# Kernel tuning notes

Hardware: AMD Instinct MI355X
Metric: run time of the kernel (lower is better)

The kernel has to match this reference:

```python
import jax, jax.numpy as jnp
import numpy as np

B, T, D, M, H = 1, 256, 512, 64, 8
HD = D // H              # head_dim = 64
IN = 2 * HD + 2 * M      # crossing_net input dim = 256
HID = D // 2             # crossing_net hidden = 256


def setup_inputs() -> dict:
    key = jax.random.key(0)
    ks = jax.random.split(key, 14)
    s = 0.02
    return {
        "x": jax.random.normal(ks[0], (B, T, D), jnp.float32),
        "coords": jax.random.normal(ks[1], (B, T, M), jnp.float32),
        "Wq": jax.random.normal(ks[2], (D, D), jnp.float32) * s,
        "Wk": jax.random.normal(ks[3], (D, D), jnp.float32) * s,
        "Wv": jax.random.normal(ks[4], (D, D), jnp.float32) * s,
        "Wo": jax.random.normal(ks[5], (D, D), jnp.float32) * s,
        "W1": jax.random.normal(ks[6], (IN, HID), jnp.float32) * s,
        "b1": jnp.zeros((HID,), jnp.float32),
        "W2": jax.random.normal(ks[7], (HID, 2), jnp.float32) * s,
        "b2": jnp.zeros((2,), jnp.float32),
        "W3": jax.random.normal(ks[8], (D, D), jnp.float32) * s,
        "b3": jnp.zeros((D,), jnp.float32),
        "W4": jax.random.normal(ks[9], (D, D), jnp.float32) * s,
        "b4": jnp.zeros((D,), jnp.float32),
    }


def reference(x, coords, Wq, Wk, Wv, Wo, W1, b1, W2, b2, W3, b3, W4, b4):
    b, t, d = x.shape
    m = coords.shape[-1]
    hd = d // H
    # projections -> (B, H, T, HD)
    q = (x @ Wq).reshape(b, t, H, hd).transpose(0, 2, 1, 3)
    k = (x @ Wk).reshape(b, t, H, hd).transpose(0, 2, 1, 3)
    v = (x @ Wv).reshape(b, t, H, hd).transpose(0, 2, 1, 3)
    # crossing_net layer1 on concat([q_i, k_j, c_i, c_j]) decomposes by blocks of W1:
    W1q, W1k = W1[:hd], W1[hd:2 * hd]
    W1ci, W1cj = W1[2 * hd:2 * hd + m], W1[2 * hd + m:]
    a_i = jnp.einsum('bhid,df->bhif', q, W1q) + jnp.einsum('bim,mf->bif', coords, W1ci)[:, None]
    a_j = jnp.einsum('bhjd,df->bhjf', k, W1k) + jnp.einsum('bjm,mf->bjf', coords, W1cj)[:, None] + b1
    # (B,H,T,T,HID) pairwise hidden, then layer2 -> 2 logits
    h = jax.nn.silu(a_i[:, :, :, None, :] + a_j[:, :, None, :, :])
    z = jnp.einsum('bhijf,fc->bhijc', h, W2) + b2
    crossings = jax.nn.softmax(z, axis=-1)            # (B,H,T,T,2)
    linking = crossings[..., 0] - crossings[..., 1]   # (B,H,T,T)
    scores = linking / np.float32(np.sqrt(hd))
    causal = jnp.triu(jnp.ones((t, t), bool), 1)
    scores = jnp.where(causal, -jnp.inf, scores)
    attn = jax.nn.softmax(scores, axis=-1)
    out = jnp.einsum('bhij,bhjd->bhid', attn, v)
    out = out.transpose(0, 2, 1, 3).reshape(b, t, d)
    out = jax.nn.silu(out @ W3 + b3) @ W4 + b4        # invariant_net
    out = out @ Wo                                    # to_out
    writhe = linking.sum(axis=(-1, -2))               # (B,H)
    linking_mean = jnp.abs(linking).mean()
    return out, writhe, linking_mean
```

## Files before the change

kernel.cpp:

```cpp
#include <hip/hip_runtime.h>
#include <math.h>

#define T_ 256
#define D_ 512
#define M_ 64
#define H_ 8
#define HD_ 64
#define HID_ 256


__global__ __launch_bounds__(256) void mm32_kernel(
    const float* __restrict__ A, const float* __restrict__ B,
    float* __restrict__ C, const float* __restrict__ bias, int act)
{
    __shared__ __align__(16) float As[32][36];
    __shared__ __align__(16) float Bs[32][36];

    const int tid = threadIdx.x;
    const int tx = tid & 15, ty = tid >> 4;
    const int row0 = blockIdx.y * 32, col0 = blockIdx.x * 32;
    const int r4 = tid >> 3, c4 = tid & 7;

    float acc00 = 0.f, acc01 = 0.f, acc10 = 0.f, acc11 = 0.f;

    for (int k0 = 0; k0 < D_; k0 += 32) {
        *(float4*)&As[r4][c4 * 4] = *(const float4*)(A + (long)(row0 + r4) * D_ + k0 + c4 * 4);
        *(float4*)&Bs[r4][c4 * 4] = *(const float4*)(B + (long)(k0 + r4) * D_ + col0 + c4 * 4);
        __syncthreads();
        #pragma unroll
        for (int kk = 0; kk < 32; ++kk) {
            float a0 = As[ty * 2 + 0][kk];
            float a1 = As[ty * 2 + 1][kk];
            float b0 = Bs[kk][tx * 2 + 0];
            float b1 = Bs[kk][tx * 2 + 1];
            acc00 = fmaf(a0, b0, acc00); acc01 = fmaf(a0, b1, acc01);
            acc10 = fmaf(a1, b0, acc10); acc11 = fmaf(a1, b1, acc11);
        }
        __syncthreads();
    }

    float accs[2][2] = {{acc00, acc01}, {acc10, acc11}};
    #pragma unroll
    for (int ii = 0; ii < 2; ++ii) {
        #pragma unroll
        for (int jj = 0; jj < 2; ++jj) {
            int r = row0 + ty * 2 + ii, c = col0 + tx * 2 + jj;
            float v = accs[ii][jj];
            if (bias) v += bias[c];
            if (act)  v = v * __builtin_amdgcn_rcpf(1.f + __expf(-v));
            C[(long)r * D_ + c] = v;
        }
    }
}

__global__ __launch_bounds__(256) void qkv_kernel(
    const float* __restrict__ x,
    const float* __restrict__ Wq, const float* __restrict__ Wk,
    const float* __restrict__ Wv, float* __restrict__ y)
{
    __shared__ __align__(16) float As[32][36];
    __shared__ __align__(16) float Bs[32][36];

    const int z = blockIdx.z;
    const float* W = (z == 0) ? Wq : (z == 1) ? Wk : Wv;
    float* C = y + (long)z * (T_ * D_);

    const int tid = threadIdx.x;
    const int tx = tid & 15, ty = tid >> 4;
    const int row0 = blockIdx.y * 32, col0 = blockIdx.x * 32;
    const int r4 = tid >> 3, c4 = tid & 7;

    float acc00 = 0.f, acc01 = 0.f, acc10 = 0.f, acc11 = 0.f;

    for (int k0 = 0; k0 < D_; k0 += 32) {
        *(float4*)&As[r4][c4 * 4] = *(const float4*)(x + (long)(row0 + r4) * D_ + k0 + c4 * 4);
        *(float4*)&Bs[r4][c4 * 4] = *(const float4*)(W + (long)(k0 + r4) * D_ + col0 + c4 * 4);
        __syncthreads();
        #pragma unroll
        for (int kk = 0; kk < 32; ++kk) {
            float a0 = As[ty * 2 + 0][kk];
            float a1 = As[ty * 2 + 1][kk];
            float b0 = Bs[kk][tx * 2 + 0];
            float b1 = Bs[kk][tx * 2 + 1];
            acc00 = fmaf(a0, b0, acc00); acc01 = fmaf(a0, b1, acc01);
            acc10 = fmaf(a1, b0, acc10); acc11 = fmaf(a1, b1, acc11);
        }
        __syncthreads();
    }
    C[(long)(row0 + ty * 2 + 0) * D_ + col0 + tx * 2 + 0] = acc00;
    C[(long)(row0 + ty * 2 + 0) * D_ + col0 + tx * 2 + 1] = acc01;
    C[(long)(row0 + ty * 2 + 1) * D_ + col0 + tx * 2 + 0] = acc10;
    C[(long)(row0 + ty * 2 + 1) * D_ + col0 + tx * 2 + 1] = acc11;
}

__global__ __launch_bounds__(256) void aiaj_kernel(
    const float* __restrict__ y, const float* __restrict__ coords,
    const float* __restrict__ W1, const float* __restrict__ b1,
    float* __restrict__ abuf)
{
    __shared__ __align__(16) float As[32][36];
    __shared__ __align__(16) float Bs[32][36];

    const int z = blockIdx.z;
    const int sel = z >> 3, h = z & 7;
    const float* Ay = y + (long)sel * (T_ * D_) + h * HD_;
    float* C = abuf + (long)z * (T_ * HID_);

    const int tid = threadIdx.x;
    const int tx = tid & 15, ty = tid >> 4;
    const int row0 = blockIdx.y * 32, col0 = blockIdx.x * 32;
    const int r4 = tid >> 3, c4 = tid & 7;

    float acc00 = 0.f, acc01 = 0.f, acc10 = 0.f, acc11 = 0.f;

    for (int k0 = 0; k0 < 128; k0 += 32) {
        if (k0 < 64) {
            *(float4*)&As[r4][c4 * 4] =
                *(const float4*)(Ay + (long)(row0 + r4) * D_ + k0 + c4 * 4);
            *(float4*)&Bs[r4][c4 * 4] =
                *(const float4*)(W1 + (long)(sel * 64 + k0 + r4) * HID_ + col0 + c4 * 4);
        } else {
            *(float4*)&As[r4][c4 * 4] =
                *(const float4*)(coords + (long)(row0 + r4) * M_ + (k0 - 64) + c4 * 4);
            *(float4*)&Bs[r4][c4 * 4] =
                *(const float4*)(W1 + (long)(128 + 64 * sel + k0 - 64 + r4) * HID_ + col0 + c4 * 4);
        }
        __syncthreads();
        #pragma unroll
        for (int kk = 0; kk < 32; ++kk) {
            float a0 = As[ty * 2 + 0][kk];
            float a1 = As[ty * 2 + 1][kk];
            float b0 = Bs[kk][tx * 2 + 0];
            float b1 = Bs[kk][tx * 2 + 1];
            acc00 = fmaf(a0, b0, acc00); acc01 = fmaf(a0, b1, acc01);
            acc10 = fmaf(a1, b0, acc10); acc11 = fmaf(a1, b1, acc11);
        }
        __syncthreads();
    }
    const int c0 = col0 + tx * 2, r0 = row0 + ty * 2;
    float bb0 = (sel == 1) ? b1[c0 + 0] : 0.f;
    float bb1 = (sel == 1) ? b1[c0 + 1] : 0.f;
    C[(long)(r0 + 0) * HID_ + c0 + 0] = acc00 + bb0;
    C[(long)(r0 + 0) * HID_ + c0 + 1] = acc01 + bb1;
    C[(long)(r0 + 1) * HID_ + c0 + 0] = acc10 + bb0;
    C[(long)(r0 + 1) * HID_ + c0 + 1] = acc11 + bb1;
}

#define SILU_ACC(acc, w, aa, bb) \
    { float t_ = (aa) + (bb); \
      float sg_ = __builtin_amdgcn_rcpf(1.f + __expf(-t_)); \
      acc = fmaf((w) * t_, sg_, acc); }

__global__ __launch_bounds__(256) void pairwise_kernel(
    const float* __restrict__ a_i, const float* __restrict__ a_j,
    const float* __restrict__ W2, float* __restrict__ pb)
{
    const int jt = blockIdx.x, it = blockIdx.y, hs = blockIdx.z;
    const int h = hs >> 1, fb = (hs & 1) * 128;
    const int t = threadIdx.x;

    __shared__ __align__(16) float ai_s[32][132];
    __shared__ __align__(16) float aj_s[32][132];
    __shared__ __align__(16) float w2d[128];

    if (t < 128) w2d[t] = W2[(fb + t) * 2 + 0] - W2[(fb + t) * 2 + 1];

    const float* aib = a_i + ((long)h * T_ + it * 32) * HID_ + fb;
    const float* ajb = a_j + ((long)h * T_ + jt * 32) * HID_ + fb;
    #pragma unroll
    for (int l = 0; l < 4; ++l) {
        int idx = t + l * 256;
        int r = idx >> 5, c4 = idx & 31;
        *(float4*)&ai_s[r][c4 * 4] = *(const float4*)(aib + (long)r * HID_ + c4 * 4);
        *(float4*)&aj_s[r][c4 * 4] = *(const float4*)(ajb + (long)r * HID_ + c4 * 4);
    }
    __syncthreads();

    const int ty = t >> 4, tx = t & 15;
    float s00 = 0.f, s01 = 0.f, s10 = 0.f, s11 = 0.f;

    #pragma unroll
    for (int fc = 0; fc < 2; ++fc) {
        const float* wp = &w2d[fc * 64];
        #pragma unroll 4
        for (int f4 = 0; f4 < 16; ++f4) {
            float4 a0 = *(const float4*)&ai_s[ty][fc * 64 + f4 * 4];
            float4 a1 = *(const float4*)&ai_s[ty + 16][fc * 64 + f4 * 4];
            float4 c0 = *(const float4*)&aj_s[tx][fc * 64 + f4 * 4];
            float4 c1 = *(const float4*)&aj_s[tx + 16][fc * 64 + f4 * 4];
            float4 w  = *(const float4*)&wp[f4 * 4];
            SILU_ACC(s00, w.x, a0.x, c0.x); SILU_ACC(s01, w.x, a0.x, c1.x);
            SILU_ACC(s10, w.x, a1.x, c0.x); SILU_ACC(s11, w.x, a1.x, c1.x);
            SILU_ACC(s00, w.y, a0.y, c0.y); SILU_ACC(s01, w.y, a0.y, c1.y);
            SILU_ACC(s10, w.y, a1.y, c0.y); SILU_ACC(s11, w.y, a1.y, c1.y);
            SILU_ACC(s00, w.z, a0.z, c0.z); SILU_ACC(s01, w.z, a0.z, c1.z);
            SILU_ACC(s10, w.z, a1.z, c0.z); SILU_ACC(s11, w.z, a1.z, c1.z);
            SILU_ACC(s00, w.w, a0.w, c0.w); SILU_ACC(s01, w.w, a0.w, c1.w);
            SILU_ACC(s10, w.w, a1.w, c0.w); SILU_ACC(s11, w.w, a1.w, c1.w);
        }
    }

    const int gi0 = it * 32 + ty, gi1 = gi0 + 16;
    const int gj0 = jt * 32 + tx, gj1 = gj0 + 16;
    float* pbh = pb + (long)hs * (T_ * T_);
    pbh[(long)gi0 * T_ + gj0] = s00;
    pbh[(long)gi0 * T_ + gj1] = s01;
    pbh[(long)gi1 * T_ + gj0] = s10;
    pbh[(long)gi1 * T_ + gj1] = s11;
}

__global__ __launch_bounds__(512) void attn_kernel(
    const float* __restrict__ pb, const float* __restrict__ yv,
    const float* __restrict__ b2, float* __restrict__ o,
    float* __restrict__ parts)
{
    const int i = blockIdx.x, t = threadIdx.x;
    const int w = t >> 6, lane = t & 63;

    __shared__ float p[8][256];
    __shared__ float psc[8];

    const float b2d = b2[0] - b2[1];

    const float* pb0 = pb + ((long)(2 * w + 0) * T_ + i) * T_;
    const float* pb1 = pb + ((long)(2 * w + 1) * T_ + i) * T_;
    float sv[4];
    float mx = -1e30f, wsum = 0.f, asum = 0.f;
    #pragma unroll
    for (int r = 0; r < 4; ++r) {
        int j = lane + r * 64;
        float s = pb0[j] + pb1[j] + b2d;
        float as = fabsf(s);
        float e = __expf(-as);
        float tv = (1.f - e) * __builtin_amdgcn_rcpf(1.f + e);
        float lk = (s < 0.f) ? -tv : tv;
        wsum += lk; asum += fabsf(lk);
        float sc = (j <= i) ? lk * 0.125f : -1e30f;
        sv[r] = sc; mx = fmaxf(mx, sc);
    }
    #pragma unroll
    for (int off = 32; off > 0; off >>= 1) mx = fmaxf(mx, __shfl_xor(mx, off));
    float sum = 0.f;
    #pragma unroll
    for (int r = 0; r < 4; ++r) {
        int j = lane + r * 64;
        float e = (j <= i) ? __expf(sv[r] - mx) : 0.f;
        p[w][j] = e; sum += e;
    }
    #pragma unroll
    for (int off = 32; off > 0; off >>= 1) {
        sum  += __shfl_xor(sum, off);
        wsum += __shfl_xor(wsum, off);
        asum += __shfl_xor(asum, off);
    }
    if (lane == 0) {
        psc[w] = __builtin_amdgcn_rcpf(sum);
        parts[((long)i * 8 + w) * 2 + 0] = wsum;
        parts[((long)i * 8 + w) * 2 + 1] = asum;
    }
    __syncthreads();

    const float pinv = psc[w];
    const float* vb = yv + t;
    float a0 = 0.f, a1 = 0.f, a2 = 0.f, a3 = 0.f;
    int j = 0;
    for (; j + 3 <= i; j += 4) {
        a0 = fmaf(p[w][j + 0], vb[(long)(j + 0) * D_], a0);
        a1 = fmaf(p[w][j + 1], vb[(long)(j + 1) * D_], a1);
        a2 = fmaf(p[w][j + 2], vb[(long)(j + 2) * D_], a2);
        a3 = fmaf(p[w][j + 3], vb[(long)(j + 3) * D_], a3);
    }
    for (; j <= i; ++j) a0 = fmaf(p[w][j], vb[(long)j * D_], a0);
    o[(long)i * D_ + t] = ((a0 + a1) + (a2 + a3)) * pinv;
}

__global__ __launch_bounds__(64) void tail_kernel(
    const float* __restrict__ parts, float* __restrict__ tailo)
{
    const int lane = threadIdx.x;
    if (lane < 8) {
        float wsum = 0.f;
        for (int i = 0; i < 256; ++i) wsum += parts[((long)i * 8 + lane) * 2 + 0];
        tailo[lane] = wsum;
    }
    float a = 0.f;
    for (int idx = lane; idx < 2048; idx += 64) a += parts[(long)idx * 2 + 1];
    #pragma unroll
    for (int off = 32; off > 0; off >>= 1) a += __shfl_xor(a, off);
    if (lane == 0) tailo[8] = a / (float)(H_ * T_ * T_);
}

extern "C" void kernel_launch(void* const* d_in, const int* in_sizes, int n_in,
                              void* d_out, int out_size, void* d_ws, size_t ws_size,
                              hipStream_t stream)
{
    const float* x      = (const float*)d_in[0];
    const float* coords = (const float*)d_in[1];
    const float* Wq     = (const float*)d_in[2];
    const float* Wk     = (const float*)d_in[3];
    const float* Wv     = (const float*)d_in[4];
    const float* Wo     = (const float*)d_in[5];
    const float* W1     = (const float*)d_in[6];
    const float* b1     = (const float*)d_in[7];
    const float* W2     = (const float*)d_in[8];
    const float* b2     = (const float*)d_in[9];
    const float* W3     = (const float*)d_in[10];
    const float* b3     = (const float*)d_in[11];
    const float* W4     = (const float*)d_in[12];
    const float* b4     = (const float*)d_in[13];
    float* out = (float*)d_out;

    float* ws = (float*)d_ws;
    float* y     = ws;
    float* ai    = ws + 393216;
    float* aj    = ws + 917504;
    float* pb    = ws + 1441792;
    float* o     = ws + 2490368;
    float* g1    = ws + 2621440;
    float* g2    = ws + 2752512;
    float* parts = ws + 2883584;

    qkv_kernel<<<dim3(16, 8, 3), dim3(256), 0, stream>>>(x, Wq, Wk, Wv, y);

    aiaj_kernel<<<dim3(8, 8, 16), dim3(256), 0, stream>>>(y, coords, W1, b1, ai);

    pairwise_kernel<<<dim3(8, 8, 16), dim3(256), 0, stream>>>(ai, aj, W2, pb);

    attn_kernel<<<dim3(T_), dim3(512), 0, stream>>>(pb, y + 2 * (T_ * D_), b2, o, parts);

    mm32_kernel<<<dim3(16, 8), dim3(256), 0, stream>>>(o,  W3, g1,  b3, 1);
    mm32_kernel<<<dim3(16, 8), dim3(256), 0, stream>>>(g1, W4, g2,  b4, 0);
    mm32_kernel<<<dim3(16, 8), dim3(256), 0, stream>>>(g2, Wo, out, nullptr, 0);

    tail_kernel<<<dim3(1), dim3(64), 0, stream>>>(parts, out + 131072);
}
```

Before: 137.1 us.

## Split pairwise feature dim four ways, split-K epilogue GEMMs, fuse tail reduction

Result: faster. 119.4 us (-12.9%).

```diff
diff --git a/kernel.cpp b/kernel.cpp
--- a/kernel.cpp
+++ b/kernel.cpp
@@ -8,50 +8,6 @@
 #define HD_ 64
 #define HID_ 256
 
-
-__global__ __launch_bounds__(256) void mm32_kernel(
-    const float* __restrict__ A, const float* __restrict__ B,
-    float* __restrict__ C, const float* __restrict__ bias, int act)
-{
-    __shared__ __align__(16) float As[32][36];
-    __shared__ __align__(16) float Bs[32][36];
-
-    const int tid = threadIdx.x;
-    const int tx = tid & 15, ty = tid >> 4;
-    const int row0 = blockIdx.y * 32, col0 = blockIdx.x * 32;
-    const int r4 = tid >> 3, c4 = tid & 7;
-
-    float acc00 = 0.f, acc01 = 0.f, acc10 = 0.f, acc11 = 0.f;
-
-    for (int k0 = 0; k0 < D_; k0 += 32) {
-        *(float4*)&As[r4][c4 * 4] = *(const float4*)(A + (long)(row0 + r4) * D_ + k0 + c4 * 4);
-        *(float4*)&Bs[r4][c4 * 4] = *(const float4*)(B + (long)(k0 + r4) * D_ + col0 + c4 * 4);
-        __syncthreads();
-        #pragma unroll
-        for (int kk = 0; kk < 32; ++kk) {
-            float a0 = As[ty * 2 + 0][kk];
-            float a1 = As[ty * 2 + 1][kk];
-            float b0 = Bs[kk][tx * 2 + 0];
-            float b1 = Bs[kk][tx * 2 + 1];
-            acc00 = fmaf(a0, b0, acc00); acc01 = fmaf(a0, b1, acc01);
-            acc10 = fmaf(a1, b0, acc10); acc11 = fmaf(a1, b1, acc11);
-        }
-        __syncthreads();
-    }
-
-    float accs[2][2] = {{acc00, acc01}, {acc10, acc11}};
-    #pragma unroll
-    for (int ii = 0; ii < 2; ++ii) {
-        #pragma unroll
-        for (int jj = 0; jj < 2; ++jj) {
-            int r = row0 + ty * 2 + ii, c = col0 + tx * 2 + jj;
-            float v = accs[ii][jj];
-            if (bias) v += bias[c];
-            if (act)  v = v * __builtin_amdgcn_rcpf(1.f + __expf(-v));
-            C[(long)r * D_ + c] = v;
-        }
-    }
-}
 
 __global__ __launch_bounds__(256) void qkv_kernel(
     const float* __restrict__ x,
@@ -156,21 +112,21 @@
     const float* __restrict__ W2, float* __restrict__ pb)
 {
     const int jt = blockIdx.x, it = blockIdx.y, hs = blockIdx.z;
-    const int h = hs >> 1, fb = (hs & 1) * 128;
+    const int h = hs >> 2, fb = (hs & 3) * 64;
     const int t = threadIdx.x;
 
-    __shared__ __align__(16) float ai_s[32][132];
-    __shared__ __align__(16) float aj_s[32][132];
-    __shared__ __align__(16) float w2d[128];
-
-    if (t < 128) w2d[t] = W2[(fb + t) * 2 + 0] - W2[(fb + t) * 2 + 1];
+    __shared__ __align__(16) float ai_s[32][68];
+    __shared__ __align__(16) float aj_s[32][68];
+    __shared__ __align__(16) float w2d[64];
+
+    if (t < 64) w2d[t] = W2[(fb + t) * 2 + 0] - W2[(fb + t) * 2 + 1];
 
     const float* aib = a_i + ((long)h * T_ + it * 32) * HID_ + fb;
     const float* ajb = a_j + ((long)h * T_ + jt * 32) * HID_ + fb;
     #pragma unroll
-    for (int l = 0; l < 4; ++l) {
+    for (int l = 0; l < 2; ++l) {
         int idx = t + l * 256;
-        int r = idx >> 5, c4 = idx & 31;
+        int r = idx >> 4, c4 = idx & 15;
         *(float4*)&ai_s[r][c4 * 4] = *(const float4*)(aib + (long)r * HID_ + c4 * 4);
         *(float4*)&aj_s[r][c4 * 4] = *(const float4*)(ajb + (long)r * HID_ + c4 * 4);
     }
@@ -179,25 +135,21 @@
     const int ty = t >> 4, tx = t & 15;
     float s00 = 0.f, s01 = 0.f, s10 = 0.f, s11 = 0.f;
 
-    #pragma unroll
-    for (int fc = 0; fc < 2; ++fc) {
-        const float* wp = &w2d[fc * 64];
-        #pragma unroll 4
-        for (int f4 = 0; f4 < 16; ++f4) {
-            float4 a0 = *(const float4*)&ai_s[ty][fc * 64 + f4 * 4];
-            float4 a1 = *(const float4*)&ai_s[ty + 16][fc * 64 + f4 * 4];
-            float4 c0 = *(const float4*)&aj_s[tx][fc * 64 + f4 * 4];
-            float4 c1 = *(const float4*)&aj_s[tx + 16][fc * 64 + f4 * 4];
-            float4 w  = *(const float4*)&wp[f4 * 4];
-            SILU_ACC(s00, w.x, a0.x, c0.x); SILU_ACC(s01, w.x, a0.x, c1.x);
-            SILU_ACC(s10, w.x, a1.x, c0.x); SILU_ACC(s11, w.x, a1.x, c1.x);
-            SILU_ACC(s00, w.y, a0.y, c0.y); SILU_ACC(s01, w.y, a0.y, c1.y);
-            SILU_ACC(s10, w.y, a1.y, c0.y); SILU_ACC(s11, w.y, a1.y, c1.y);
-            SILU_ACC(s00, w.z, a0.z, c0.z); SILU_ACC(s01, w.z, a0.z, c1.z);
-            SILU_ACC(s10, w.z, a1.z, c0.z); SILU_ACC(s11, w.z, a1.z, c1.z);
-            SILU_ACC(s00, w.w, a0.w, c0.w); SILU_ACC(s01, w.w, a0.w, c1.w);
-            SILU_ACC(s10, w.w, a1.w, c0.w); SILU_ACC(s11, w.w, a1.w, c1.w);
-        }
+    #pragma unroll 4
+    for (int f4 = 0; f4 < 16; ++f4) {
+        float4 a0 = *(const float4*)&ai_s[ty][f4 * 4];
+        float4 a1 = *(const float4*)&ai_s[ty + 16][f4 * 4];
+        float4 c0 = *(const float4*)&aj_s[tx][f4 * 4];
+        float4 c1 = *(const float4*)&aj_s[tx + 16][f4 * 4];
+        float4 w  = *(const float4*)&w2d[f4 * 4];
+        SILU_ACC(s00, w.x, a0.x, c0.x); SILU_ACC(s01, w.x, a0.x, c1.x);
+        SILU_ACC(s10, w.x, a1.x, c0.x); SILU_ACC(s11, w.x, a1.x, c1.x);
+        SILU_ACC(s00, w.y, a0.y, c0.y); SILU_ACC(s01, w.y, a0.y, c1.y);
+        SILU_ACC(s10, w.y, a1.y, c0.y); SILU_ACC(s11, w.y, a1.y, c1.y);
+        SILU_ACC(s00, w.z, a0.z, c0.z); SILU_ACC(s01, w.z, a0.z, c1.z);
+        SILU_ACC(s10, w.z, a1.z, c0.z); SILU_ACC(s11, w.z, a1.z, c1.z);
+        SILU_ACC(s00, w.w, a0.w, c0.w); SILU_ACC(s01, w.w, a0.w, c1.w);
+        SILU_ACC(s10, w.w, a1.w, c0.w); SILU_ACC(s11, w.w, a1.w, c1.w);
     }
 
     const int gi0 = it * 32 + ty, gi1 = gi0 + 16;
@@ -222,14 +174,16 @@
 
     const float b2d = b2[0] - b2[1];
 
-    const float* pb0 = pb + ((long)(2 * w + 0) * T_ + i) * T_;
-    const float* pb1 = pb + ((long)(2 * w + 1) * T_ + i) * T_;
+    const float* pb0 = pb + ((long)(4 * w + 0) * T_ + i) * T_;
+    const float* pb1 = pb + ((long)(4 * w + 1) * T_ + i) * T_;
+    const float* pb2 = pb + ((long)(4 * w + 2) * T_ + i) * T_;
+    const float* pb3 = pb + ((long)(4 * w + 3) * T_ + i) * T_;
     float sv[4];
     float mx = -1e30f, wsum = 0.f, asum = 0.f;
     #pragma unroll
     for (int r = 0; r < 4; ++r) {
         int j = lane + r * 64;
-        float s = pb0[j] + pb1[j] + b2d;
+        float s = ((pb0[j] + pb1[j]) + (pb2[j] + pb3[j])) + b2d;
         float as = fabsf(s);
         float e = __expf(-as);
         float tv = (1.f - e) * __builtin_amdgcn_rcpf(1.f + e);
@@ -263,31 +217,170 @@
     const float pinv = psc[w];
     const float* vb = yv + t;
     float a0 = 0.f, a1 = 0.f, a2 = 0.f, a3 = 0.f;
+    float a4 = 0.f, a5 = 0.f, a6 = 0.f, a7 = 0.f;
     int j = 0;
-    for (; j + 3 <= i; j += 4) {
+    for (; j + 7 <= i; j += 8) {
         a0 = fmaf(p[w][j + 0], vb[(long)(j + 0) * D_], a0);
         a1 = fmaf(p[w][j + 1], vb[(long)(j + 1) * D_], a1);
         a2 = fmaf(p[w][j + 2], vb[(long)(j + 2) * D_], a2);
         a3 = fmaf(p[w][j + 3], vb[(long)(j + 3) * D_], a3);
+        a4 = fmaf(p[w][j + 4], vb[(long)(j + 4) * D_], a4);
+        a5 = fmaf(p[w][j + 5], vb[(long)(j + 5) * D_], a5);
+        a6 = fmaf(p[w][j + 6], vb[(long)(j + 6) * D_], a6);
+        a7 = fmaf(p[w][j + 7], vb[(long)(j + 7) * D_], a7);
     }
     for (; j <= i; ++j) a0 = fmaf(p[w][j], vb[(long)j * D_], a0);
-    o[(long)i * D_ + t] = ((a0 + a1) + (a2 + a3)) * pinv;
-}
-
-__global__ __launch_bounds__(64) void tail_kernel(
+    o[(long)i * D_ + t] = (((a0 + a1) + (a2 + a3)) + ((a4 + a5) + (a6 + a7))) * pinv;
+}
+
+__global__ __launch_bounds__(256) void epA_kernel(
+    const float* __restrict__ o, const float* __restrict__ W3,
+    float* __restrict__ hbuf)
+{
+    __shared__ __align__(16) float As[32][36];
+    __shared__ __align__(16) float Bs[32][36];
+
+    const int z = blockIdx.z;
+    float* C = hbuf + (long)z * (T_ * D_);
+    const int tid = threadIdx.x;
+    const int tx = tid & 15, ty = tid >> 4;
+    const int row0 = blockIdx.y * 32, col0 = blockIdx.x * 32;
+    const int r4 = tid >> 3, c4 = tid & 7;
+
+    float acc00 = 0.f, acc01 = 0.f, acc10 = 0.f, acc11 = 0.f;
+
+    for (int k0 = z * 256; k0 < z * 256 + 256; k0 += 32) {
+        *(float4*)&As[r4][c4 * 4] = *(const float4*)(o + (long)(row0 + r4) * D_ + k0 + c4 * 4);
+        *(float4*)&Bs[r4][c4 * 4] = *(const float4*)(W3 + (long)(k0 + r4) * D_ + col0 + c4 * 4);
+        __syncthreads();
+        #pragma unroll
+        for (int kk = 0; kk < 32; ++kk) {
+            float a0 = As[ty * 2 + 0][kk];
+            float a1 = As[ty * 2 + 1][kk];
+            float b0 = Bs[kk][tx * 2 + 0];
+            float b1 = Bs[kk][tx * 2 + 1];
+            acc00 = fmaf(a0, b0, acc00); acc01 = fmaf(a0, b1, acc01);
+            acc10 = fmaf(a1, b0, acc10); acc11 = fmaf(a1, b1, acc11);
+        }
+        __syncthreads();
+    }
+    C[(long)(row0 + ty * 2 + 0) * D_ + col0 + tx * 2 + 0] = acc00;
+    C[(long)(row0 + ty * 2 + 0) * D_ + col0 + tx * 2 + 1] = acc01;
+    C[(long)(row0 + ty * 2 + 1) * D_ + col0 + tx * 2 + 0] = acc10;
+    C[(long)(row0 + ty * 2 + 1) * D_ + col0 + tx * 2 + 1] = acc11;
+}
+
+__global__ __launch_bounds__(256) void epB_kernel(
+    const float* __restrict__ hbuf, const float* __restrict__ b3,
+    const float* __restrict__ W4, float* __restrict__ gbuf)
+{
+    __shared__ __align__(16) float As[32][36];
+    __shared__ __align__(16) float Bs[32][36];
+
+    const int z = blockIdx.z;
+    const float* h0 = hbuf;
+    const float* h1 = hbuf + (T_ * D_);
+    float* C = gbuf + (long)z * (T_ * D_);
+    const int tid = threadIdx.x;
+    const int tx = tid & 15, ty = tid >> 4;
+    const int row0 = blockIdx.y * 32, col0 = blockIdx.x * 32;
+    const int r4 = tid >> 3, c4 = tid & 7;
+
+    float acc00 = 0.f, acc01 = 0.f, acc10 = 0.f, acc11 = 0.f;
+
+    for (int k0 = z * 256; k0 < z * 256 + 256; k0 += 32) {
+        {
+            long off = (long)(row0 + r4) * D_ + k0 + c4 * 4;
+            float4 v0 = *(const float4*)(h0 + off);
+            float4 v1 = *(const float4*)(h1 + off);
+            float4 bb = *(const float4*)(b3 + k0 + c4 * 4);
+            float4 g;
+            g.x = v0.x + v1.x + bb.x; g.y = v0.y + v1.y + bb.y;
+            g.z = v0.z + v1.z + bb.z; g.w = v0.w + v1.w + bb.w;
+            g.x = g.x * __builtin_amdgcn_rcpf(1.f + __expf(-g.x));
+            g.y = g.y * __builtin_amdgcn_rcpf(1.f + __expf(-g.y));
+            g.z = g.z * __builtin_amdgcn_rcpf(1.f + __expf(-g.z));
+            g.w = g.w * __builtin_amdgcn_rcpf(1.f + __expf(-g.w));
+            *(float4*)&As[r4][c4 * 4] = g;
+        }
+        *(float4*)&Bs[r4][c4 * 4] = *(const float4*)(W4 + (long)(k0 + r4) * D_ + col0 + c4 * 4);
+        __syncthreads();
+        #pragma unroll
+        for (int kk = 0; kk < 32; ++kk) {
+            float a0 = As[ty * 2 + 0][kk];
+            float a1 = As[ty * 2 + 1][kk];
+            float b0 = Bs[kk][tx * 2 + 0];
+            float b1 = Bs[kk][tx * 2 + 1];
+            acc00 = fmaf(a0, b0, acc00); acc01 = fmaf(a0, b1, acc01);
+            acc10 = fmaf(a1, b0, acc10); acc11 = fmaf(a1, b1, acc11);
+        }
+        __syncthreads();
+    }
+    C[(long)(row0 + ty * 2 + 0) * D_ + col0 + tx * 2 + 0] = acc00;
+    C[(long)(row0 + ty * 2 + 0) * D_ + col0 + tx * 2 + 1] = acc01;
+    C[(long)(row0 + ty * 2 + 1) * D_ + col0 + tx * 2 + 0] = acc10;
+    C[(long)(row0 + ty * 2 + 1) * D_ + col0 + tx * 2 + 1] = acc11;
+}
+
+__global__ __launch_bounds__(256) void epC_kernel(
+    const float* __restrict__ gbuf, const float* __restrict__ b4,
+    const float* __restrict__ Wo, float* __restrict__ out,
     const float* __restrict__ parts, float* __restrict__ tailo)
 {
-    const int lane = threadIdx.x;
-    if (lane < 8) {
-        float wsum = 0.f;
-        for (int i = 0; i < 256; ++i) wsum += parts[((long)i * 8 + lane) * 2 + 0];
-        tailo[lane] = wsum;
-    }
-    float a = 0.f;
-    for (int idx = lane; idx < 2048; idx += 64) a += parts[(long)idx * 2 + 1];
-    #pragma unroll
-    for (int off = 32; off > 0; off >>= 1) a += __shfl_xor(a, off);
-    if (lane == 0) tailo[8] = a / (float)(H_ * T_ * T_);
+    __shared__ __align__(16) float As[32][36];
+    __shared__ __align__(16) float Bs[32][36];
+
+    const float* g0 = gbuf;
+    const float* g1 = gbuf + (T_ * D_);
+    const int tid = threadIdx.x;
+    const int tx = tid & 15, ty = tid >> 4;
+    const int row0 = blockIdx.y * 32, col0 = blockIdx.x * 32;
+    const int r4 = tid >> 3, c4 = tid & 7;
+
+    float acc00 = 0.f, acc01 = 0.f, acc10 = 0.f, acc11 = 0.f;
+
+    for (int k0 = 0; k0 < D_; k0 += 32) {
+        {
+            long off = (long)(row0 + r4) * D_ + k0 + c4 * 4;
+            float4 v0 = *(const float4*)(g0 + off);
+            float4 v1 = *(const float4*)(g1 + off);
+            float4 bb = *(const float4*)(b4 + k0 + c4 * 4);
+            float4 g;
+            g.x = v0.x + v1.x + bb.x; g.y = v0.y + v1.y + bb.y;
+            g.z = v0.z + v1.z + bb.z; g.w = v0.w + v1.w + bb.w;
+            *(float4*)&As[r4][c4 * 4] = g;
+        }
+        *(float4*)&Bs[r4][c4 * 4] = *(const float4*)(Wo + (long)(k0 + r4) * D_ + col0 + c4 * 4);
+        __syncthreads();
+        #pragma unroll
+        for (int kk = 0; kk < 32; ++kk) {
+            float a0 = As[ty * 2 + 0][kk];
+            float a1 = As[ty * 2 + 1][kk];
+            float b0 = Bs[kk][tx * 2 + 0];
+            float b1 = Bs[kk][tx * 2 + 1];
+            acc00 = fmaf(a0, b0, acc00); acc01 = fmaf(a0, b1, acc01);
+            acc10 = fmaf(a1, b0, acc10); acc11 = fmaf(a1, b1, acc11);
+        }
+        __syncthreads();
+    }
+    out[(long)(row0 + ty * 2 + 0) * D_ + col0 + tx * 2 + 0] = acc00;
+    out[(long)(row0 + ty * 2 + 0) * D_ + col0 + tx * 2 + 1] = acc01;
+    out[(long)(row0 + ty * 2 + 1) * D_ + col0 + tx * 2 + 0] = acc10;
+    out[(long)(row0 + ty * 2 + 1) * D_ + col0 + tx * 2 + 1] = acc11;
+
+    if (blockIdx.x == 0 && blockIdx.y == 0 && tid < 64) {
+        const int lane = tid;
+        if (lane < 8) {
+            float wsum = 0.f;
+            for (int i = 0; i < 256; ++i) wsum += parts[((long)i * 8 + lane) * 2 + 0];
+            tailo[lane] = wsum;
+        }
+        float a = 0.f;
+        for (int idx = lane; idx < 2048; idx += 64) a += parts[(long)idx * 2 + 1];
+        #pragma unroll
+        for (int off = 32; off > 0; off >>= 1) a += __shfl_xor(a, off);
+        if (lane == 0) tailo[8] = a / (float)(H_ * T_ * T_);
+    }
 }
 
 extern "C" void kernel_launch(void* const* d_in, const int* in_sizes, int n_in,
@@ -315,22 +408,20 @@
     float* ai    = ws + 393216;
     float* aj    = ws + 917504;
     float* pb    = ws + 1441792;
-    float* o     = ws + 2490368;
-    float* g1    = ws + 2621440;
-    float* g2    = ws + 2752512;
-    float* parts = ws + 2883584;
+    float* o     = ws + 3538944;
+    float* hb    = ws + 3670016;
+    float* gb    = ws + 3932160;
+    float* parts = ws + 4194304;
 
     qkv_kernel<<<dim3(16, 8, 3), dim3(256), 0, stream>>>(x, Wq, Wk, Wv, y);
 
     aiaj_kernel<<<dim3(8, 8, 16), dim3(256), 0, stream>>>(y, coords, W1, b1, ai);
 
-    pairwise_kernel<<<dim3(8, 8, 16), dim3(256), 0, stream>>>(ai, aj, W2, pb);
+    pairwise_kernel<<<dim3(8, 8, 32), dim3(256), 0, stream>>>(ai, aj, W2, pb);
 
     attn_kernel<<<dim3(T_), dim3(512), 0, stream>>>(pb, y + 2 * (T_ * D_), b2, o, parts);
 
-    mm32_kernel<<<dim3(16, 8), dim3(256), 0, stream>>>(o,  W3, g1,  b3, 1);
-    mm32_kernel<<<dim3(16, 8), dim3(256), 0, stream>>>(g1, W4, g2,  b4, 0);
-    mm32_kernel<<<dim3(16, 8), dim3(256), 0, stream>>>(g2, Wo, out, nullptr, 0);
-
-    tail_kernel<<<dim3(1), dim3(64), 0, stream>>>(parts, out + 131072);
-}
+    epA_kernel<<<dim3(16, 8, 2), dim3(256), 0, stream>>>(o, W3, hb);
+    epB_kernel<<<dim3(16, 8, 2), dim3(256), 0, stream>>>(hb, b3, W4, gb);
+    epC_kernel<<<dim3(16, 8), dim3(256), 0, stream>>>(gb, b4, Wo, out, parts, out + 131072);
+}
```
